# Kernel tuning notes

Measured on AMD Instinct MI355X. Metric: run time of the kernel, lower is better.

Reference implementation:

```python
import jax, jax.numpy as jnp
import numpy as np

B, TX, TY, C, H = 2, 1024, 4096, 768, 12
D = C // H  # head_dim = 64


def setup_inputs() -> dict:
    key = jax.random.key(0)
    ks = jax.random.split(key, 7)
    x = jax.random.normal(ks[0], (B, TX, C), dtype=jnp.float32)
    y = jax.random.normal(ks[1], (B, TY, C), dtype=jnp.float32)
    # sorted float timestamps in [0, TY]
    x_t = jnp.sort(jax.random.uniform(ks[2], (B, TX), dtype=jnp.float32) * TY, axis=-1)
    y_t = jnp.sort(jax.random.uniform(ks[3], (B, TY), dtype=jnp.float32) * TY, axis=-1)
    y_t = y_t.at[:, 0].set(0.0)  # guarantee every query sees >=1 valid key
    Wq = jax.random.normal(ks[4], (C, C), dtype=jnp.float32) * 0.02
    Wkv = jax.random.normal(ks[5], (C, 2 * C), dtype=jnp.float32) * 0.02
    Wproj = jax.random.normal(ks[6], (C, C), dtype=jnp.float32) * 0.02
    # RotaryEmbedding(dim=D, learned_freq=True): init values are the standard inv freqs
    inv_freq = 1.0 / (10000.0 ** (jnp.arange(0, D, 2, dtype=jnp.float32) / D))
    return {"x": x, "x_t": x_t, "y": y, "y_t": y_t, "dist": 512, "min_dist": 0,
            "Wq": Wq, "Wkv": Wkv, "Wproj": Wproj, "inv_freq": inv_freq}


def _rotate_half(t):
    # interleaved pair rotation: (x1, x2) -> (-x2, x1)
    p = t.reshape(t.shape[:-1] + (-1, 2))
    x1, x2 = p[..., 0], p[..., 1]
    return jnp.stack((-x2, x1), axis=-1).reshape(t.shape)


def _apply_rope(t, pos, inv_freq):
    # t: (B,H,T,D), pos: (B,T), inv_freq: (D/2,)
    f = pos[:, None, :, None] * inv_freq          # (B,1,T,D/2)
    f = jnp.repeat(f, 2, axis=-1)                 # (B,1,T,D) interleaved
    return t * jnp.cos(f) + _rotate_half(t) * jnp.sin(f)


def reference(x, x_t, y, y_t, dist, min_dist, Wq, Wkv, Wproj, inv_freq):
    q = (x @ Wq).reshape(B, TX, H, D).transpose(0, 2, 1, 3)   # (B,H,TX,D)
    kv = y @ Wkv
    k = kv[..., :C].reshape(B, TY, H, D).transpose(0, 2, 1, 3)
    v = kv[..., C:].reshape(B, TY, H, D).transpose(0, 2, 1, 3)
    q = _apply_rope(q, x_t, inv_freq)
    k = _apply_rope(k, y_t, inv_freq)
    # time-window mask: valid iff (x_t - min_dist) >= y_t and (x_t - min_dist) <= y_t + dist
    xt = (x_t - min_dist)[:, :, None]             # (B,TX,1)
    yt = y_t[:, None, :]                          # (B,1,TY)
    mask = (xt >= yt) & (xt <= yt + dist)         # (B,TX,TY)
    scores = jnp.einsum('bhqd,bhkd->bhqk', q, k) / jnp.sqrt(jnp.float32(D))
    scores = jnp.where(mask[:, None, :, :], scores, -jnp.inf)
    attn = jax.nn.softmax(scores, axis=-1)
    out = jnp.einsum('bhqk,bhkd->bhqd', attn, v)
    out = out.transpose(0, 2, 1, 3).reshape(B, TX, C)
    return out @ Wproj
```

## Files before the change

kernel.cpp:

```cpp
#include <hip/hip_runtime.h>
#include <hip/hip_bf16.h>
#include <math.h>

#define B_ 2
#define TX_ 1024
#define TY_ 4096
#define C_ 768
#define H_ 12
#define D_ 64
#define NSPLIT 2
#define R_ (B_ * H_ * TX_)

typedef __bf16 bf16x8 __attribute__((ext_vector_type(8)));
typedef float floatx4 __attribute__((ext_vector_type(4)));

__device__ __forceinline__ void async_copy16(const void* g, void* l) {
    __builtin_amdgcn_global_load_lds(
        (const __attribute__((address_space(1))) unsigned int*)g,
        (__attribute__((address_space(3))) unsigned int*)l,
        16, 0, 0);
}

__device__ __forceinline__ void async_copy4(const void* g, void* l) {
    __builtin_amdgcn_global_load_lds(
        (const __attribute__((address_space(1))) unsigned int*)g,
        (__attribute__((address_space(3))) unsigned int*)l,
        4, 0, 0);
}

__device__ __forceinline__ bf16x8 cvt8(const float* s) {
    bf16x8 r;
#pragma unroll
    for (int i = 0; i < 8; i++) r[i] = (__bf16)s[i];
    return r;
}

__global__ __launch_bounds__(256)
void prep(const float* __restrict__ x,  __bf16* __restrict__ xb,
          const float* __restrict__ y,  __bf16* __restrict__ yb,
          const float* __restrict__ Wq, __bf16* __restrict__ Wqt,
          const float* __restrict__ Wkv,__bf16* __restrict__ Wkvt,
          const float* __restrict__ Wpr,__bf16* __restrict__ Wprt)
{
    __shared__ float tile[32][33];
    const int bid = blockIdx.x;
    if (bid >= 2304) {
        const int cb = bid - 2304;
        const float* src; __bf16* dst; size_t base;
        if (cb < 768) { src = x; dst = xb; base = (size_t)cb * 2048; }
        else          { src = y; dst = yb; base = (size_t)(cb - 768) * 2048; }
        const size_t i = base + threadIdx.x * 8;
        float4 v0 = *(const float4*)(src + i);
        float4 v1 = *(const float4*)(src + i + 4);
        bf16x8 p;
        p[0] = (__bf16)v0.x; p[1] = (__bf16)v0.y; p[2] = (__bf16)v0.z; p[3] = (__bf16)v0.w;
        p[4] = (__bf16)v1.x; p[5] = (__bf16)v1.y; p[6] = (__bf16)v1.z; p[7] = (__bf16)v1.w;
        *(bf16x8*)(dst + i) = p;
        return;
    }
    const int bxr = bid % 96;
    const int byr = bid / 96;
    const float* W; __bf16* Wt; int N, nb; float scale = 1.0f;
    if (bxr < 24)      { W = Wq;  Wt = Wqt;  N = C_;     nb = bxr;      scale = 0.125f; }
    else if (bxr < 72) { W = Wkv; Wt = Wkvt; N = 2 * C_; nb = bxr - 24; }
    else               { W = Wpr; Wt = Wprt; N = C_;     nb = bxr - 72; }
    const int bx = nb * 32;
    const int by = byr * 32;
    const int tx = threadIdx.x & 31, ty = threadIdx.x >> 5;
#pragma unroll
    for (int i = 0; i < 4; i++)
        tile[ty + i * 8][tx] = W[(size_t)(by + ty + i * 8) * N + bx + tx];
    __syncthreads();
#pragma unroll
    for (int i = 0; i < 4; i++)
        Wt[(size_t)(bx + ty + i * 8) * C_ + by + tx] =
            (__bf16)(tile[tx][ty + i * 8] * scale);
}

__global__ __launch_bounds__(256)
void gemm_qkv(const __bf16* __restrict__ xb, const __bf16* __restrict__ Wqt,
              const __bf16* __restrict__ yb, const __bf16* __restrict__ Wkvt,
              __bf16* __restrict__ Qbh, __bf16* __restrict__ Kbh,
              __bf16* __restrict__ Vtb,
              const float* __restrict__ x_t, const float* __restrict__ y_t,
              const float* __restrict__ inv_freq)
{
    const int bid = (blockIdx.x & 7) * 216 + (blockIdx.x >> 3);
    const bool isQ = (bid < 192);
    const __bf16* A; const __bf16* Bt; const float* t_arr;
    int row0, n0, T, TSH;
    if (isQ) {
        A = xb; Bt = Wqt; t_arr = x_t;
        row0 = (bid / 6) * 64; n0 = (bid % 6) * 128; T = TX_; TSH = 10;
    } else {
        const int r = bid - 192;
        A = yb; Bt = Wkvt; t_arr = y_t;
        row0 = (r / 12) * 64; n0 = (r % 12) * 128; T = TY_; TSH = 12;
    }
    const bool isV = (!isQ) && (n0 >= C_);

    __shared__ __align__(16) float smem_f[9216];
    __bf16* smem_b = (__bf16*)smem_f;

    const int tid  = threadIdx.x;
    const int wave = tid >> 6;
    const int lane = tid & 63;
    const int m16  = lane & 15;
    const int quad = lane >> 4;
    const int wm   = wave >> 1;
    const int wn   = wave & 1;

    floatx4 acc[2][4];
#pragma unroll
    for (int i = 0; i < 2; i++)
#pragma unroll
        for (int j = 0; j < 4; j++) acc[i][j] = (floatx4){0.f, 0.f, 0.f, 0.f};

    const int eA = wave * 512 + lane * 8;
    const int srA = eA >> 5, scA = eA & 31;
    int srB[2], scB[2];
#pragma unroll
    for (int j = 0; j < 2; j++) {
        const int e = j * 2048 + wave * 512 + lane * 8;
        srB[j] = e >> 5; scB[j] = e & 31;
    }

    auto stage = [&](int chunk, int buf) {
        const int kk = chunk * 32;
        async_copy16(A + (size_t)(row0 + srA) * C_ + (kk + scA),
                     (char*)smem_f + buf * 12288 + wave * 1024);
#pragma unroll
        for (int j = 0; j < 2; j++)
            async_copy16(Bt + (size_t)(n0 + srB[j]) * C_ + (kk + scB[j]),
                         (char*)smem_f + buf * 12288 + 4096 + j * 4096 + wave * 1024);
    };

    stage(0, 0);
    stage(1, 1);

    int cur = 0;
    for (int t = 0; t < 24; ++t) {
        if (t < 23) asm volatile("s_waitcnt vmcnt(3)" ::: "memory");
        else        asm volatile("s_waitcnt vmcnt(0)" ::: "memory");
        __builtin_amdgcn_s_barrier();
        asm volatile("" ::: "memory");

        if (t + 2 < 24) {
            int nb = cur + 2; if (nb >= 3) nb -= 3;
            stage(t + 2, nb);
        }

        const __bf16* As = smem_b + cur * 6144;
        const __bf16* Bs = As + 2048;
        bf16x8 af[2], bfr[4];
#pragma unroll
        for (int i = 0; i < 2; i++)
            af[i] = *(const bf16x8*)(As + (size_t)(wm * 32 + i * 16 + m16) * 32 + quad * 8);
#pragma unroll
        for (int j = 0; j < 4; j++)
            bfr[j] = *(const bf16x8*)(Bs + (size_t)(wn * 64 + j * 16 + m16) * 32 + quad * 8);
#pragma unroll
        for (int i = 0; i < 2; i++)
#pragma unroll
            for (int j = 0; j < 4; j++)
                acc[i][j] = __builtin_amdgcn_mfma_f32_16x16x32_bf16(af[i], bfr[j], acc[i][j], 0, 0, 0);

        cur = (cur == 2) ? 0 : cur + 1;
    }

    const int STR = 132;
    float* fs = smem_f;

#pragma unroll
    for (int i = 0; i < 2; i++) {
        __syncthreads();
#pragma unroll
        for (int j = 0; j < 4; j++) {
            const int col_l = wn * 64 + j * 16 + m16;
#pragma unroll
            for (int r = 0; r < 4; r++) {
                const int row_l = quad * 4 + r;
                float v = acc[i][j][r];
                if (!isV) {
                    const float vp = __shfl_xor(v, 1);
                    const int row = row0 + wm * 32 + i * 16 + row_l;
                    const int cc = (n0 + col_l) & (D_ - 1);
                    const float fr = t_arr[row] * inv_freq[cc >> 1];
                    const float sn = __sinf(fr), cs = __cosf(fr);
                    v = (m16 & 1) ? (v * cs + vp * sn) : (v * cs - vp * sn);
                }
                fs[(wm * 16 + row_l) * STR + col_l] = v;
            }
        }
        __syncthreads();

        if (!isV) {
            __bf16* outb = isQ ? Qbh : Kbh;
            const int r32 = tid >> 3;
            const int lane8 = tid & 7;
            const int grow = row0 + (r32 >> 4) * 32 + i * 16 + (r32 & 15);
            const int bb = grow >> TSH;
            const int rk = grow & (T - 1);
            const int h  = (n0 >> 6) + (lane8 >> 2);
            const int d0 = (lane8 & 3) * 16;
            __bf16* gp = outb + ((size_t)(bb * H_ + h) * T + rk) * 64 + d0;
            const float* sp = &fs[r32 * STR + lane8 * 16];
            *(bf16x8*)gp       = cvt8(sp);
            *(bf16x8*)(gp + 8) = cvt8(sp + 8);
        } else {
            const int dcol = tid >> 1;
            const int g16  = tid & 1;
            const int h  = ((n0 - C_) >> 6) + (dcol >> 6);
            const int dd = dcol & 63;
            const int kbase = row0 + g16 * 32 + i * 16;
            const int bb  = kbase >> 12;
            const int kin = kbase & (TY_ - 1);
            float tmp[16];
#pragma unroll
            for (int jj = 0; jj < 16; jj++)
                tmp[jj] = fs[(g16 * 16 + jj) * STR + dcol];
            __bf16* gp = Vtb + ((size_t)(bb * H_ + h) * 64 + dd) * TY_ + kin;
            *(bf16x8*)gp       = cvt8(tmp);
            *(bf16x8*)(gp + 8) = cvt8(tmp + 8);
        }
    }
}

__global__ __launch_bounds__(256)
void attn_mfma(const __bf16* __restrict__ Qb,
               const __bf16* __restrict__ Kb,
               const __bf16* __restrict__ Vt,
               const float* __restrict__ x_t,
               const float* __restrict__ y_t,
               const int* __restrict__ dist_p,
               const int* __restrict__ min_dist_p,
               float* __restrict__ pacc,
               float* __restrict__ pml)
{
    __shared__ __align__(16) __bf16 Kc3[3 * 32 * 64];
    __shared__ __align__(16) __bf16 Vc3[3 * 64 * 32];
    __shared__ __align__(16) float  ytl[3 * 32];
    __shared__ __align__(16) __bf16 Pt[4][16 * 32];

    const int tid  = threadIdx.x;
    const int wave = tid >> 6;
    const int m16  = tid & 15;
    const int quad = (tid & 63) >> 4;
    const int qt = blockIdx.x, bh = blockIdx.y, split = blockIdx.z;
    const int b = bh / H_;
    const int qblk  = qt * 64;
    const int qbase = qblk + wave * 16;

    const float dist = (float)dist_p[0];
    const float md   = (float)min_dist_p[0];
    const float* yt = y_t + (size_t)b * TY_;
    const float* xt = x_t + (size_t)b * TX_;

    const float xtmin = xt[qblk] - md;
    const float xtmax = xt[qblk + 63] - md;
    int lo = 0, hi = TY_;
    while (lo < hi) { int mid = (lo + hi) >> 1; if (yt[mid] + dist < xtmin) lo = mid + 1; else hi = mid; }
    const int klo = lo;
    lo = 0; hi = TY_;
    while (lo < hi) { int mid = (lo + hi) >> 1; if (yt[mid] <= xtmax) lo = mid + 1; else hi = mid; }
    const int khi = lo - 1;
    const int len = khi - klo + 1;

    int k0 = klo, k1 = klo;
    if (len > 0) {
        const int cnt = (len + NSPLIT - 1) / NSPLIT;
        k0 = klo + split * cnt;
        k1 = min(k0 + cnt, klo + len);
    }
    const int nt = (k1 > k0) ? ((k1 - k0 + 31) >> 5) : 0;

    float xtq[4];
#pragma unroll
    for (int r = 0; r < 4; r++)
        xtq[r] = xt[qbase + quad * 4 + r] - md;

    const __bf16* qp = Qb + ((size_t)bh * TX_ + qbase + m16) * 64;
    const bf16x8 aq0 = *(const bf16x8*)(qp + quad * 8);
    const bf16x8 aq1 = *(const bf16x8*)(qp + 32 + quad * 8);

    float l[4];
    floatx4 o[4];
#pragma unroll
    for (int r = 0; r < 4; r++) l[r] = 0.f;
#pragma unroll
    for (int ot = 0; ot < 4; ot++) o[ot] = (floatx4){0.f, 0.f, 0.f, 0.f};

    auto stageA = [&](int c, int buf) {
        const int kc = k0 + c * 32;
        const int krow = tid >> 3;
        const int kg = min(kc + krow, TY_ - 1);
        async_copy16(Kb + ((size_t)bh * TY_ + kg) * 64 + (tid & 7) * 8,
                     (char*)Kc3 + buf * 4096 + tid * 16);
        const int d = tid >> 2;
        const int kv = min(kc + (tid & 3) * 8, TY_ - 8);
        async_copy16(Vt + ((size_t)bh * 64 + d) * TY_ + kv,
                     (char*)Vc3 + buf * 4096 + tid * 16);
        if (tid < 32) {
            const int gk = min(kc + tid, TY_ - 1);
            async_copy4(yt + gk, (char*)ytl + buf * 128 + tid * 4);
        }
    };

    if (nt > 0) stageA(0, 0);
    if (nt > 1) stageA(1, 1);

    int cur = 0;
    for (int tc = 0; tc < nt; ++tc) {
        if (tc < nt - 1) {
            if (wave == 0) asm volatile("s_waitcnt vmcnt(3)" ::: "memory");
            else           asm volatile("s_waitcnt vmcnt(2)" ::: "memory");
        } else {
            asm volatile("s_waitcnt vmcnt(0)" ::: "memory");
        }
        __builtin_amdgcn_s_barrier();
        asm volatile("" ::: "memory");

        if (tc + 2 < nt) {
            int nb = cur + 2; if (nb >= 3) nb -= 3;
            stageA(tc + 2, nb);
        }

        const int kc = k0 + tc * 32;
        const __bf16* Kc = Kc3 + cur * 2048;
        const __bf16* Vc = Vc3 + cur * 2048;
        const float yt0 = ytl[cur * 32 + m16];
        const float yt1 = ytl[cur * 32 + 16 + m16];

        const bf16x8 bk0h0 = *(const bf16x8*)(Kc + m16 * 64 + quad * 8);
        const bf16x8 bk1h0 = *(const bf16x8*)(Kc + m16 * 64 + 32 + quad * 8);
        const bf16x8 bk0h1 = *(const bf16x8*)(Kc + (16 + m16) * 64 + quad * 8);
        const bf16x8 bk1h1 = *(const bf16x8*)(Kc + (16 + m16) * 64 + 32 + quad * 8);
        floatx4 s0 = (floatx4){0.f, 0.f, 0.f, 0.f};
        floatx4 s1 = (floatx4){0.f, 0.f, 0.f, 0.f};
        s0 = __builtin_amdgcn_mfma_f32_16x16x32_bf16(aq0, bk0h0, s0, 0, 0, 0);
        s0 = __builtin_amdgcn_mfma_f32_16x16x32_bf16(aq1, bk1h0, s0, 0, 0, 0);
        s1 = __builtin_amdgcn_mfma_f32_16x16x32_bf16(aq0, bk0h1, s1, 0, 0, 0);
        s1 = __builtin_amdgcn_mfma_f32_16x16x32_bf16(aq1, bk1h1, s1, 0, 0, 0);

        const int kg0 = kc + m16;
        const int kg1 = kc + 16 + m16;
        __bf16* pt = Pt[wave];
#pragma unroll
        for (int r = 0; r < 4; r++) {
            const bool v0 = (kg0 < k1) && (xtq[r] >= yt0) && (xtq[r] <= yt0 + dist);
            const bool v1 = (kg1 < k1) && (xtq[r] >= yt1) && (xtq[r] <= yt1 + dist);
            const float p0 = v0 ? (float)(__bf16)__expf(s0[r]) : 0.f;
            const float p1 = v1 ? (float)(__bf16)__expf(s1[r]) : 0.f;
            l[r] += p0 + p1;
            pt[(quad * 4 + r) * 32 + m16]      = (__bf16)p0;
            pt[(quad * 4 + r) * 32 + 16 + m16] = (__bf16)p1;
        }
        const bf16x8 ap = *(const bf16x8*)(pt + m16 * 32 + quad * 8);
#pragma unroll
        for (int ot = 0; ot < 4; ot++) {
            const bf16x8 bv = *(const bf16x8*)(Vc + (ot * 16 + m16) * 32 + quad * 8);
            o[ot] = __builtin_amdgcn_mfma_f32_16x16x32_bf16(ap, bv, o[ot], 0, 0, 0);
        }

        cur = (cur == 2) ? 0 : cur + 1;
    }

#pragma unroll
    for (int r = 0; r < 4; r++) {
#pragma unroll
        for (int w = 1; w < 16; w <<= 1)
            l[r] += __shfl_xor(l[r], w);
    }

#pragma unroll
    for (int ot = 0; ot < 4; ot++)
#pragma unroll
        for (int r = 0; r < 4; r++) {
            const size_t gr = (size_t)bh * TX_ + qbase + quad * 4 + r;
            pacc[((size_t)split * R_ + gr) * 64 + ot * 16 + m16] = o[ot][r];
        }
    if (m16 == 0) {
#pragma unroll
        for (int r = 0; r < 4; r++) {
            const size_t gr = (size_t)bh * TX_ + qbase + quad * 4 + r;
            pml[(size_t)split * R_ + gr] = l[r];
        }
    }
}

__global__ __launch_bounds__(256)
void combine_kernel(const float* __restrict__ pacc,
                    const float* __restrict__ pml,
                    __bf16* __restrict__ O)
{
    const int d   = threadIdx.x;
    const int sub = threadIdx.y;
    const size_t r = (size_t)blockIdx.x * 4 + sub;
    const int bh  = (int)(r / TX_);
    const int txg = (int)(r % TX_);
    const int b = bh / H_, h = bh % H_;

    float L = 0.f, val = 0.f;
#pragma unroll
    for (int s = 0; s < NSPLIT; s++) {
        L   += pml[(size_t)s * R_ + r];
        val += pacc[((size_t)s * R_ + r) * 64 + d];
    }
    const float o = (L > 0.f) ? val / L : 0.f;
    O[(size_t)(b * TX_ + txg) * C_ + h * D_ + d] = (__bf16)o;
}

__global__ __launch_bounds__(256)
void gemm_proj(const __bf16* __restrict__ A,
               const __bf16* __restrict__ Bt,
               float* __restrict__ out0)
{
    const int bid = (blockIdx.x & 7) * 24 + (blockIdx.x >> 3);
    const int row0 = (bid / 6) * 64;
    const int n0   = (bid % 6) * 128;

    __shared__ __align__(16) float smem_f[12288];
    __bf16* smem_b = (__bf16*)smem_f;

    const int tid  = threadIdx.x;
    const int wave = tid >> 6;
    const int lane = tid & 63;
    const int m16  = lane & 15;
    const int quad = lane >> 4;
    const int wm   = wave >> 1;
    const int wn   = wave & 1;

    floatx4 acc[2][4];
#pragma unroll
    for (int i = 0; i < 2; i++)
#pragma unroll
        for (int j = 0; j < 4; j++) acc[i][j] = (floatx4){0.f, 0.f, 0.f, 0.f};

    const int eA = wave * 512 + lane * 8;
    const int srA = eA >> 5, scA = eA & 31;
    int srB[2], scB[2];
#pragma unroll
    for (int j = 0; j < 2; j++) {
        const int e = j * 2048 + wave * 512 + lane * 8;
        srB[j] = e >> 5; scB[j] = e & 31;
    }

    auto stage = [&](int chunk, int buf) {
        const int kk = chunk * 32;
        async_copy16(A + (size_t)(row0 + srA) * C_ + (kk + scA),
                     (char*)smem_f + buf * 12288 + wave * 1024);
#pragma unroll
        for (int j = 0; j < 2; j++)
            async_copy16(Bt + (size_t)(n0 + srB[j]) * C_ + (kk + scB[j]),
                         (char*)smem_f + buf * 12288 + 4096 + j * 4096 + wave * 1024);
    };

    stage(0, 0);
    stage(1, 1);
    stage(2, 2);

    for (int t = 0; t < 24; ++t) {
        if (t < 22)      asm volatile("s_waitcnt vmcnt(6)" ::: "memory");
        else if (t == 22) asm volatile("s_waitcnt vmcnt(3)" ::: "memory");
        else              asm volatile("s_waitcnt vmcnt(0)" ::: "memory");
        __builtin_amdgcn_s_barrier();
        asm volatile("" ::: "memory");

        if (t + 3 < 24) stage(t + 3, (t + 3) & 3);

        const __bf16* As = smem_b + (t & 3) * 6144;
        const __bf16* Bs = As + 2048;
        bf16x8 af[2], bfr[4];
#pragma unroll
        for (int i = 0; i < 2; i++)
            af[i] = *(const bf16x8*)(As + (size_t)(wm * 32 + i * 16 + m16) * 32 + quad * 8);
#pragma unroll
        for (int j = 0; j < 4; j++)
            bfr[j] = *(const bf16x8*)(Bs + (size_t)(wn * 64 + j * 16 + m16) * 32 + quad * 8);
#pragma unroll
        for (int i = 0; i < 2; i++)
#pragma unroll
            for (int j = 0; j < 4; j++)
                acc[i][j] = __builtin_amdgcn_mfma_f32_16x16x32_bf16(af[i], bfr[j], acc[i][j], 0, 0, 0);
    }

    const int STR = 132;
    float* fs = smem_f;
#pragma unroll
    for (int i = 0; i < 2; i++) {
        __syncthreads();
#pragma unroll
        for (int j = 0; j < 4; j++) {
            const int col_l = wn * 64 + j * 16 + m16;
#pragma unroll
            for (int r = 0; r < 4; r++)
                fs[(wm * 16 + quad * 4 + r) * STR + col_l] = acc[i][j][r];
        }
        __syncthreads();
        const int r32 = tid >> 3;
        const int lc  = (tid & 7) * 4;
        const int row = row0 + (r32 >> 4) * 32 + i * 16 + (r32 & 15);
        float* gp = out0 + (size_t)row * C_ + n0;
#pragma unroll
        for (int c2 = 0; c2 < 4; c2++) {
            float4 v4 = *(const float4*)&fs[r32 * STR + c2 * 32 + lc];
            *(float4*)(gp + c2 * 32 + lc) = v4;
        }
    }
}

extern "C" void kernel_launch(void* const* d_in, const int* in_sizes, int n_in,
                              void* d_out, int out_size, void* d_ws, size_t ws_size,
                              hipStream_t stream)
{
    const float* x        = (const float*)d_in[0];
    const float* x_t      = (const float*)d_in[1];
    const float* y        = (const float*)d_in[2];
    const float* y_t      = (const float*)d_in[3];
    const int*   dist     = (const int*)d_in[4];
    const int*   min_dist = (const int*)d_in[5];
    const float* Wq       = (const float*)d_in[6];
    const float* Wkv      = (const float*)d_in[7];
    const float* Wproj    = (const float*)d_in[8];
    const float* inv_freq = (const float*)d_in[9];
    float* out = (float*)d_out;

    const size_t QN = (size_t)B_ * TX_ * C_;
    const size_t KN = (size_t)B_ * TY_ * C_;

    float* ws = (float*)d_ws;
    float* pacc = ws; ws += (size_t)NSPLIT * R_ * 64;
    float* pml  = ws; ws += (size_t)NSPLIT * R_;
    __bf16* bws = (__bf16*)ws;
    __bf16* xb    = bws; bws += QN;
    __bf16* yb    = bws; bws += KN;
    __bf16* Wqt   = bws; bws += (size_t)C_ * C_;
    __bf16* Wkvt  = bws; bws += (size_t)C_ * 2 * C_;
    __bf16* Wprt  = bws; bws += (size_t)C_ * C_;
    __bf16* Ob    = bws; bws += QN;
    __bf16* Qbh   = bws; bws += QN;
    __bf16* Kbh   = bws; bws += KN;
    __bf16* Vtb   = bws; bws += KN + 128;

    prep<<<dim3(2304 + 3840), dim3(256), 0, stream>>>(
        x, xb, y, yb, Wq, Wqt, Wkv, Wkvt, Wproj, Wprt);

    gemm_qkv<<<dim3(1728), dim3(256), 0, stream>>>(
        xb, Wqt, yb, Wkvt, Qbh, Kbh, Vtb, x_t, y_t, inv_freq);

    attn_mfma<<<dim3(TX_ / 64, B_ * H_, NSPLIT), dim3(256), 0, stream>>>(
        Qbh, Kbh, Vtb, x_t, y_t, dist, min_dist, pacc, pml);

    combine_kernel<<<dim3((unsigned)(R_ / 4)), dim3(64, 4), 0, stream>>>(
        pacc, pml, Ob);

    gemm_proj<<<dim3(192), dim3(256), 0, stream>>>(
        Ob, Wprt, out);
}
```

Baseline: 181.7 us.

## Merge split-K attention into 512-thread blocks with in-LDS combine and swizzled LDS

The two key-range splits now run as two 256-thread wave groups inside one 512-thread block instead of as separate grid blocks. Their partial outputs and row sums are reduced through shared memory, and the normalized bf16 result is written directly, so the separate combine kernel and its fp32 partial buffers go away. XOR swizzles are also added to the K, V and P shared-memory layouts to reduce bank conflicts. The costs are more LDS per block, lower block count, and a barrier that makes both groups wait for the longer of the two halves.

```diff
diff --git a/kernel.cpp b/kernel.cpp
--- a/kernel.cpp
+++ b/kernel.cpp
@@ -8,7 +8,6 @@
 #define C_ 768
 #define H_ 12
 #define D_ 64
-#define NSPLIT 2
 #define R_ (B_ * H_ * TX_)
 
 typedef __bf16 bf16x8 __attribute__((ext_vector_type(8)));
@@ -226,7 +225,7 @@
     }
 }
 
-__global__ __launch_bounds__(256)
+__global__ __launch_bounds__(512)
 void attn_mfma(const __bf16* __restrict__ Qb,
                const __bf16* __restrict__ Kb,
                const __bf16* __restrict__ Vt,
@@ -234,22 +233,28 @@
                const float* __restrict__ y_t,
                const int* __restrict__ dist_p,
                const int* __restrict__ min_dist_p,
-               float* __restrict__ pacc,
-               float* __restrict__ pml)
+               __bf16* __restrict__ Ob)
 {
-    __shared__ __align__(16) __bf16 Kc3[3 * 32 * 64];
-    __shared__ __align__(16) __bf16 Vc3[3 * 64 * 32];
-    __shared__ __align__(16) float  ytl[3 * 32];
-    __shared__ __align__(16) __bf16 Pt[4][16 * 32];
+    __shared__ __align__(16) __bf16 Kc3[2][3 * 32 * 64];
+    __shared__ __align__(16) __bf16 Vc3[2][3 * 64 * 32];
+    __shared__ __align__(16) float  ytl[2][3 * 32];
+    __shared__ __align__(16) __bf16 Pt[8][16 * 32];
+    __shared__ __align__(16) float  ex_o[64][66];
+    __shared__ float ex_l[64];
 
     const int tid  = threadIdx.x;
     const int wave = tid >> 6;
-    const int m16  = tid & 15;
-    const int quad = (tid & 63) >> 4;
-    const int qt = blockIdx.x, bh = blockIdx.y, split = blockIdx.z;
+    const int g    = wave >> 2;
+    const int w4   = wave & 3;
+    const int t256 = tid & 255;
+    const int lane = tid & 63;
+    const int m16  = lane & 15;
+    const int quad = lane >> 4;
+    const int qt = blockIdx.x, bh = blockIdx.y;
     const int b = bh / H_;
+    const int h = bh % H_;
     const int qblk  = qt * 64;
-    const int qbase = qblk + wave * 16;
+    const int qbase = qblk + w4 * 16;
 
     const float dist = (float)dist_p[0];
     const float md   = (float)min_dist_p[0];
@@ -266,13 +271,16 @@
     const int khi = lo - 1;
     const int len = khi - klo + 1;
 
-    int k0 = klo, k1 = klo;
+    int k0g = klo, k1g = klo, nt0 = 0, nt1 = 0;
     if (len > 0) {
-        const int cnt = (len + NSPLIT - 1) / NSPLIT;
-        k0 = klo + split * cnt;
-        k1 = min(k0 + cnt, klo + len);
-    }
-    const int nt = (k1 > k0) ? ((k1 - k0 + 31) >> 5) : 0;
+        const int cnt = (len + 1) >> 1;
+        nt0 = (cnt + 31) >> 5;
+        nt1 = (len - cnt + 31) >> 5;
+        if (g == 0) { k0g = klo;       k1g = klo + cnt; }
+        else        { k0g = klo + cnt; k1g = klo + len; }
+    }
+    const int ntg   = (g == 0) ? nt0 : nt1;
+    const int ntmax = (nt0 > nt1) ? nt0 : nt1;
 
     float xtq[4];
 #pragma unroll
@@ -290,51 +298,57 @@
 #pragma unroll
     for (int ot = 0; ot < 4; ot++) o[ot] = (floatx4){0.f, 0.f, 0.f, 0.f};
 
+    const int ksrc = (((t256 & 7) ^ ((t256 >> 3) & 7))) * 8;
+    const int vchk = (t256 & 3) ^ ((t256 >> 3) & 3);
+
     auto stageA = [&](int c, int buf) {
-        const int kc = k0 + c * 32;
-        const int krow = tid >> 3;
+        const int kc = k0g + c * 32;
+        const int krow = t256 >> 3;
         const int kg = min(kc + krow, TY_ - 1);
-        async_copy16(Kb + ((size_t)bh * TY_ + kg) * 64 + (tid & 7) * 8,
-                     (char*)Kc3 + buf * 4096 + tid * 16);
-        const int d = tid >> 2;
-        const int kv = min(kc + (tid & 3) * 8, TY_ - 8);
+        async_copy16(Kb + ((size_t)bh * TY_ + kg) * 64 + ksrc,
+                     (char*)Kc3[g] + buf * 4096 + t256 * 16);
+        const int d = t256 >> 2;
+        const int kv = min(kc + vchk * 8, TY_ - 8);
         async_copy16(Vt + ((size_t)bh * 64 + d) * TY_ + kv,
-                     (char*)Vc3 + buf * 4096 + tid * 16);
-        if (tid < 32) {
-            const int gk = min(kc + tid, TY_ - 1);
-            async_copy4(yt + gk, (char*)ytl + buf * 128 + tid * 4);
+                     (char*)Vc3[g] + buf * 4096 + t256 * 16);
+        if (t256 < 32) {
+            const int gk = min(kc + t256, TY_ - 1);
+            async_copy4(yt + gk, (char*)ytl[g] + buf * 128 + t256 * 4);
         }
     };
 
-    if (nt > 0) stageA(0, 0);
-    if (nt > 1) stageA(1, 1);
+    if (ntg > 0) stageA(0, 0);
+    if (ntg > 1) stageA(1, 1);
+
+    const int sk = m16 & 7;
+    const int sv = (m16 >> 1) & 3;
 
     int cur = 0;
-    for (int tc = 0; tc < nt; ++tc) {
-        if (tc < nt - 1) {
-            if (wave == 0) asm volatile("s_waitcnt vmcnt(3)" ::: "memory");
-            else           asm volatile("s_waitcnt vmcnt(2)" ::: "memory");
+    for (int tc = 0; tc < ntmax; ++tc) {
+        if (tc < ntmax - 1) {
+            if (w4 == 0) asm volatile("s_waitcnt vmcnt(3)" ::: "memory");
+            else         asm volatile("s_waitcnt vmcnt(2)" ::: "memory");
         } else {
             asm volatile("s_waitcnt vmcnt(0)" ::: "memory");
         }
         __builtin_amdgcn_s_barrier();
         asm volatile("" ::: "memory");
 
-        if (tc + 2 < nt) {
+        if (tc + 2 < ntg) {
             int nb = cur + 2; if (nb >= 3) nb -= 3;
             stageA(tc + 2, nb);
         }
 
-        const int kc = k0 + tc * 32;
-        const __bf16* Kc = Kc3 + cur * 2048;
-        const __bf16* Vc = Vc3 + cur * 2048;
-        const float yt0 = ytl[cur * 32 + m16];
-        const float yt1 = ytl[cur * 32 + 16 + m16];
-
-        const bf16x8 bk0h0 = *(const bf16x8*)(Kc + m16 * 64 + quad * 8);
-        const bf16x8 bk1h0 = *(const bf16x8*)(Kc + m16 * 64 + 32 + quad * 8);
-        const bf16x8 bk0h1 = *(const bf16x8*)(Kc + (16 + m16) * 64 + quad * 8);
-        const bf16x8 bk1h1 = *(const bf16x8*)(Kc + (16 + m16) * 64 + 32 + quad * 8);
+        const int kc = k0g + tc * 32;
+        const __bf16* Kc = Kc3[g] + cur * 2048;
+        const __bf16* Vc = Vc3[g] + cur * 2048;
+        const float yt0 = ytl[g][cur * 32 + m16];
+        const float yt1 = ytl[g][cur * 32 + 16 + m16];
+
+        const bf16x8 bk0h0 = *(const bf16x8*)(Kc + m16 * 64        + ((quad       ^ sk) * 8));
+        const bf16x8 bk1h0 = *(const bf16x8*)(Kc + m16 * 64        + (((4 + quad) ^ sk) * 8));
+        const bf16x8 bk0h1 = *(const bf16x8*)(Kc + (16 + m16) * 64 + ((quad       ^ sk) * 8));
+        const bf16x8 bk1h1 = *(const bf16x8*)(Kc + (16 + m16) * 64 + (((4 + quad) ^ sk) * 8));
         floatx4 s0 = (floatx4){0.f, 0.f, 0.f, 0.f};
         floatx4 s1 = (floatx4){0.f, 0.f, 0.f, 0.f};
         s0 = __builtin_amdgcn_mfma_f32_16x16x32_bf16(aq0, bk0h0, s0, 0, 0, 0);
@@ -347,18 +361,20 @@
         __bf16* pt = Pt[wave];
 #pragma unroll
         for (int r = 0; r < 4; r++) {
-            const bool v0 = (kg0 < k1) && (xtq[r] >= yt0) && (xtq[r] <= yt0 + dist);
-            const bool v1 = (kg1 < k1) && (xtq[r] >= yt1) && (xtq[r] <= yt1 + dist);
+            const bool v0 = (kg0 < k1g) && (xtq[r] >= yt0) && (xtq[r] <= yt0 + dist);
+            const bool v1 = (kg1 < k1g) && (xtq[r] >= yt1) && (xtq[r] <= yt1 + dist);
             const float p0 = v0 ? (float)(__bf16)__expf(s0[r]) : 0.f;
             const float p1 = v1 ? (float)(__bf16)__expf(s1[r]) : 0.f;
             l[r] += p0 + p1;
-            pt[(quad * 4 + r) * 32 + m16]      = (__bf16)p0;
-            pt[(quad * 4 + r) * 32 + 16 + m16] = (__bf16)p1;
-        }
-        const bf16x8 ap = *(const bf16x8*)(pt + m16 * 32 + quad * 8);
+            const int prow = quad * 4 + r;
+            const int sp = (prow >> 1) & 3;
+            pt[prow * 32 + (((m16 >> 3) ^ sp) * 8)       + (m16 & 7)] = (__bf16)p0;
+            pt[prow * 32 + ((((m16 >> 3) + 2) ^ sp) * 8) + (m16 & 7)] = (__bf16)p1;
+        }
+        const bf16x8 ap = *(const bf16x8*)(pt + m16 * 32 + ((quad ^ sv) * 8));
 #pragma unroll
         for (int ot = 0; ot < 4; ot++) {
-            const bf16x8 bv = *(const bf16x8*)(Vc + (ot * 16 + m16) * 32 + quad * 8);
+            const bf16x8 bv = *(const bf16x8*)(Vc + (ot * 16 + m16) * 32 + ((quad ^ sv) * 8));
             o[ot] = __builtin_amdgcn_mfma_f32_16x16x32_bf16(ap, bv, o[ot], 0, 0, 0);
         }
 
@@ -372,42 +388,44 @@
             l[r] += __shfl_xor(l[r], w);
     }
 
-#pragma unroll
-    for (int ot = 0; ot < 4; ot++)
-#pragma unroll
-        for (int r = 0; r < 4; r++) {
-            const size_t gr = (size_t)bh * TX_ + qbase + quad * 4 + r;
-            pacc[((size_t)split * R_ + gr) * 64 + ot * 16 + m16] = o[ot][r];
-        }
-    if (m16 == 0) {
-#pragma unroll
-        for (int r = 0; r < 4; r++) {
-            const size_t gr = (size_t)bh * TX_ + qbase + quad * 4 + r;
-            pml[(size_t)split * R_ + gr] = l[r];
-        }
-    }
-}
-
-__global__ __launch_bounds__(256)
-void combine_kernel(const float* __restrict__ pacc,
-                    const float* __restrict__ pml,
-                    __bf16* __restrict__ O)
-{
-    const int d   = threadIdx.x;
-    const int sub = threadIdx.y;
-    const size_t r = (size_t)blockIdx.x * 4 + sub;
-    const int bh  = (int)(r / TX_);
-    const int txg = (int)(r % TX_);
-    const int b = bh / H_, h = bh % H_;
-
-    float L = 0.f, val = 0.f;
-#pragma unroll
-    for (int s = 0; s < NSPLIT; s++) {
-        L   += pml[(size_t)s * R_ + r];
-        val += pacc[((size_t)s * R_ + r) * 64 + d];
-    }
-    const float o = (L > 0.f) ? val / L : 0.f;
-    O[(size_t)(b * TX_ + txg) * C_ + h * D_ + d] = (__bf16)o;
+    if (g == 1) {
+#pragma unroll
+        for (int ot = 0; ot < 4; ot++)
+#pragma unroll
+            for (int r = 0; r < 4; r++)
+                ex_o[w4 * 16 + quad * 4 + r][ot * 16 + m16] = o[ot][r];
+        if (m16 == 0) {
+#pragma unroll
+            for (int r = 0; r < 4; r++)
+                ex_l[w4 * 16 + quad * 4 + r] = l[r];
+        }
+    }
+    __syncthreads();
+    if (g == 0) {
+#pragma unroll
+        for (int ot = 0; ot < 4; ot++)
+#pragma unroll
+            for (int r = 0; r < 4; r++)
+                ex_o[w4 * 16 + quad * 4 + r][ot * 16 + m16] += o[ot][r];
+        if (m16 == 0) {
+#pragma unroll
+            for (int r = 0; r < 4; r++)
+                ex_l[w4 * 16 + quad * 4 + r] += l[r];
+        }
+    }
+    __syncthreads();
+
+    {
+        const int q  = tid >> 3;
+        const int d0 = (tid & 7) * 8;
+        const float L = ex_l[q];
+        const float inv = (L > 0.f) ? 1.f / L : 0.f;
+        float tmp[8];
+#pragma unroll
+        for (int j = 0; j < 8; j++) tmp[j] = ex_o[q][d0 + j] * inv;
+        __bf16* gp = Ob + ((size_t)(b * TX_ + qblk + q)) * C_ + h * 64 + d0;
+        *(bf16x8*)gp = cvt8(tmp);
+    }
 }
 
 __global__ __launch_bounds__(256)
@@ -460,7 +478,7 @@
     stage(2, 2);
 
     for (int t = 0; t < 24; ++t) {
-        if (t < 22)      asm volatile("s_waitcnt vmcnt(6)" ::: "memory");
+        if (t < 22)       asm volatile("s_waitcnt vmcnt(6)" ::: "memory");
         else if (t == 22) asm volatile("s_waitcnt vmcnt(3)" ::: "memory");
         else              asm volatile("s_waitcnt vmcnt(0)" ::: "memory");
         __builtin_amdgcn_s_barrier();
@@ -528,10 +546,7 @@
     const size_t QN = (size_t)B_ * TX_ * C_;
     const size_t KN = (size_t)B_ * TY_ * C_;
 
-    float* ws = (float*)d_ws;
-    float* pacc = ws; ws += (size_t)NSPLIT * R_ * 64;
-    float* pml  = ws; ws += (size_t)NSPLIT * R_;
-    __bf16* bws = (__bf16*)ws;
+    __bf16* bws = (__bf16*)d_ws;
     __bf16* xb    = bws; bws += QN;
     __bf16* yb    = bws; bws += KN;
     __bf16* Wqt   = bws; bws += (size_t)C_ * C_;
@@ -548,11 +563,8 @@
     gemm_qkv<<<dim3(1728), dim3(256), 0, stream>>>(
         xb, Wqt, yb, Wkvt, Qbh, Kbh, Vtb, x_t, y_t, inv_freq);
 
-    attn_mfma<<<dim3(TX_ / 64, B_ * H_, NSPLIT), dim3(256), 0, stream>>>(
-        Qbh, Kbh, Vtb, x_t, y_t, dist, min_dist, pacc, pml);
-
-    combine_kernel<<<dim3((unsigned)(R_ / 4)), dim3(64, 4), 0, stream>>>(
-        pacc, pml, Ob);
+    attn_mfma<<<dim3(TX_ / 64, B_ * H_), dim3(512), 0, stream>>>(
+        Qbh, Kbh, Vtb, x_t, y_t, dist, min_dist, Ob);
 
     gemm_proj<<<dim3(192), dim3(256), 0, stream>>>(
         Ob, Wprt, out);
```

After: 176.0 us. -3.1%, faster.
